# Kernel optimization log

Hardware: AMD Instinct MI355X
Metric: run time of the kernel (lower is better)

Reference implementation:

```python
import jax, jax.numpy as jnp
import numpy as np

B, T, D, H = 256, 512, 128, 256


def setup_inputs() -> dict:
    key = jax.random.key(0)
    ks = jax.random.split(key, 8)
    return {
        "x": jax.random.normal(ks[0], (B, T, D), jnp.float32),
        "m": jax.random.randint(ks[1], (B, T, D), 0, 2, jnp.int32),
        "s": jax.random.uniform(ks[2], (B, T, 1), jnp.float32),
        "kernel": jax.random.normal(ks[3], (D, 3 * H), jnp.float32) * 0.05,
        "recurrent_kernel": jax.random.normal(ks[4], (H, 3 * H), jnp.float32) * 0.05,
        "masking_kernel": jax.random.normal(ks[5], (D, 3 * H), jnp.float32) * 0.05,
        "bias": jnp.zeros((3 * H,), jnp.float32),
        "input_decay_kernel": jax.random.normal(ks[6], (D,), jnp.float32) * 0.05,
        "input_decay_bias": jnp.zeros((D,), jnp.float32),
        "hidden_decay_kernel": jax.random.normal(ks[7], (D, H), jnp.float32) * 0.05,
        "hidden_decay_bias": jnp.zeros((H,), jnp.float32),
    }


def _grud_scan(x, m, s, kernel, recurrent_kernel, masking_kernel, bias,
               input_decay_kernel, input_decay_bias,
               hidden_decay_kernel, hidden_decay_bias):
    b, t, d = x.shape
    h = recurrent_kernel.shape[0]
    mf = m.astype(x.dtype)
    mb = m > 0  # boolean mask, K.switch semantics
    # mask projection is h-independent -> hoist the big GEMM out of the scan
    mproj = jnp.einsum('btd,dk->btk', mf, masking_kernel)  # [B,T,3H]
    Kz, Kr, Kh = kernel[:, :h], kernel[:, h:2 * h], kernel[:, 2 * h:]
    Rz, Rr, Rh = recurrent_kernel[:, :h], recurrent_kernel[:, h:2 * h], recurrent_kernel[:, 2 * h:]
    bz, br, bh = bias[:h], bias[h:2 * h], bias[2 * h:]

    def step(carry, inp):
        h_tm1, x_keep, s_prev = carry
        xt, mbt, st, mpt = inp  # xt [B,D], mbt [B,D] bool, st [B,1], mpt [B,3H]
        d_t = st - s_prev  # [B,D] via broadcast
        gamma_di = jnp.exp(-jax.nn.relu(d_t * input_decay_kernel + input_decay_bias))
        gamma_dh = jnp.exp(-jax.nn.relu(d_t @ hidden_decay_kernel + hidden_decay_bias))
        x_keep_t = jnp.where(mbt, xt, x_keep)
        x_t = jnp.where(mbt, xt, gamma_di * x_keep_t)
        h_d = gamma_dh * h_tm1
        mz, mr, mh = mpt[:, :h], mpt[:, h:2 * h], mpt[:, 2 * h:]
        z_t = jax.nn.sigmoid(x_t @ Kz + h_d @ Rz + mz + bz)
        r_pre = x_t @ Kr + h_d @ Rr + mr + br  # original uses pre-activation r in hh
        hh_t = jnp.tanh(x_t @ Kh + (r_pre * h_d) @ Rh + mh + bh)
        h_t = z_t * h_tm1 + (1.0 - z_t) * hh_t
        s_keep = jnp.where(mbt, jnp.broadcast_to(st, s_prev.shape), s_prev)
        return (h_t, x_keep_t, s_keep), h_t

    init = (jnp.zeros((b, h), x.dtype), jnp.zeros((b, d), x.dtype), jnp.zeros((b, d), x.dtype))
    xs = (jnp.swapaxes(x, 0, 1), jnp.swapaxes(mb, 0, 1),
          jnp.swapaxes(s, 0, 1), jnp.swapaxes(mproj, 0, 1))
    _, hs = jax.lax.scan(step, init, xs)  # hs: [T,B,H]
    return jnp.swapaxes(hs, 0, 1)  # [B,T,H]


def reference(x, m, s, kernel, recurrent_kernel, masking_kernel, bias,
              input_decay_kernel, input_decay_bias,
              hidden_decay_kernel, hidden_decay_bias):
    return _grud_scan(x, m, s, kernel, recurrent_kernel, masking_kernel, bias,
                      input_decay_kernel, input_decay_bias,
                      hidden_decay_kernel, hidden_decay_bias)
```

## Files before the change

kernel.cpp:

```cpp
#include <hip/hip_runtime.h>
#include <hip/hip_bf16.h>
#include <cstdint>


#define Bsz 256
#define Tsz 512
#define Dsz 128
#define Hsz 256
#define BT  (Bsz * Tsz)
#define N3H 768

typedef __attribute__((ext_vector_type(8))) short   short8;
typedef __attribute__((ext_vector_type(8))) __bf16  bf16x8;
typedef __attribute__((ext_vector_type(4))) float   f32x4;

__device__ __forceinline__ unsigned short f2bf(float f) {
    union { float f; unsigned u; } v; v.f = f;
    unsigned r = v.u + 0x7fffu + ((v.u >> 16) & 1u);
    return (unsigned short)(r >> 16);
}
__device__ __forceinline__ float b2f(unsigned short u) {
    union { unsigned u; float f; } v; v.u = ((unsigned)u) << 16;
    return v.f;
}
__device__ __forceinline__ bf16x8 ld_frag(const unsigned short* p) {
    short8 v = *(const short8*)p;
    return __builtin_bit_cast(bf16x8, v);
}

__device__ __forceinline__ void barrier_lds() {
    asm volatile("s_waitcnt lgkmcnt(0)\n\ts_barrier" ::: "memory");
}

__global__ void k_pack(const float* __restrict__ kern, const float* __restrict__ maskk,
                       const float* __restrict__ rk,   const float* __restrict__ hdk,
                       unsigned short* __restrict__ KM_T, unsigned short* __restrict__ R_T,
                       unsigned short* __restrict__ W_T) {
    int i = blockIdx.x * 256 + threadIdx.x;
    if (i < N3H * 256) {
        int n = i >> 8, k = i & 255;
        float v = (k < 128) ? kern[k * N3H + n] : maskk[(k - 128) * N3H + n];
        KM_T[i] = f2bf(v);
        R_T[i]  = f2bf(rk[k * N3H + n]);
    } else {
        int j = i - N3H * 256;
        if (j < 256 * 128) {
            int n = j >> 7, k = j & 127;
            W_T[j] = f2bf(hdk[k * 256 + n]);
        }
    }
}

__global__ __launch_bounds__(256) void k_locf(
        const float* __restrict__ x, const int* __restrict__ m,
        const float* __restrict__ s, const float* __restrict__ wdi,
        const float* __restrict__ bdi,
        unsigned short* __restrict__ X2, unsigned short* __restrict__ Dt) {
    int gid = blockIdx.x * blockDim.x + threadIdx.x;
    int b = gid >> 7, d = gid & 127;
    float w  = wdi[d], bi = bdi[d];
    float x_keep = 0.f, s_prev = 0.f;
    const float* xb  = x + (size_t)b * Tsz * Dsz + d;
    const int*   mb_ = m + (size_t)b * Tsz * Dsz + d;
    const float* sb  = s + (size_t)b * Tsz;
    unsigned short* X2b = X2 + (size_t)b * Tsz * 256 + d;
    unsigned short* Dtb = Dt + (size_t)b * Tsz * 128 + d;
    for (int t0 = 0; t0 < Tsz; t0 += 4) {
        float xv[4], sv[4]; int mv[4];
#pragma unroll
        for (int u = 0; u < 4; u++) {
            xv[u] = xb[(size_t)(t0 + u) * Dsz];
            mv[u] = mb_[(size_t)(t0 + u) * Dsz];
            sv[u] = sb[t0 + u];
        }
#pragma unroll
        for (int u = 0; u < 4; u++) {
            int t = t0 + u;
            float dt  = sv[u] - s_prev;
            float gdi = __expf(-fmaxf(dt * w + bi, 0.f));
            bool  mbt = mv[u] > 0;
            if (mbt) x_keep = xv[u];
            float xe = mbt ? xv[u] : gdi * x_keep;
            if (mbt) s_prev = sv[u];
            X2b[(size_t)t * 256]       = f2bf(xe);
            X2b[(size_t)t * 256 + 128] = f2bf((float)mv[u]);
            Dtb[(size_t)t * 128]       = f2bf(dt);
        }
    }
}

template <int MODE, int K, int N>
__global__ __launch_bounds__(256) void k_gemm(
        const unsigned short* __restrict__ A, const unsigned short* __restrict__ Bt,
        const float* __restrict__ bias, unsigned short* __restrict__ C) {
    __shared__ unsigned short As[128][40];
    __shared__ unsigned short Bs[128][40];
    int m0 = blockIdx.x * 128, n0 = blockIdx.y * 128;
    int tid = threadIdx.x, lane = tid & 63, w = tid >> 6;
    int wm = w & 1, wn = w >> 1;
    int r15 = lane & 15, q = lane >> 4;
    int arow = tid >> 2, akg = tid & 3;
    f32x4 acc[4][4];
#pragma unroll
    for (int i = 0; i < 4; i++)
#pragma unroll
        for (int j = 0; j < 4; j++) acc[i][j] = f32x4{0.f, 0.f, 0.f, 0.f};

    for (int kk = 0; kk < K; kk += 32) {
        short8 av0 = *(const short8*)(A  + (size_t)(m0 + arow)      * K + kk + akg * 8);
        short8 av1 = *(const short8*)(A  + (size_t)(m0 + arow + 64) * K + kk + akg * 8);
        short8 bv0 = *(const short8*)(Bt + (size_t)(n0 + arow)      * K + kk + akg * 8);
        short8 bv1 = *(const short8*)(Bt + (size_t)(n0 + arow + 64) * K + kk + akg * 8);
        *(short8*)&As[arow][akg * 8]      = av0;
        *(short8*)&As[arow + 64][akg * 8] = av1;
        *(short8*)&Bs[arow][akg * 8]      = bv0;
        *(short8*)&Bs[arow + 64][akg * 8] = bv1;
        __syncthreads();
        bf16x8 af[4], bf[4];
#pragma unroll
        for (int i = 0; i < 4; i++) af[i] = ld_frag(&As[wm * 64 + i * 16 + r15][q * 8]);
#pragma unroll
        for (int j = 0; j < 4; j++) bf[j] = ld_frag(&Bs[wn * 64 + j * 16 + r15][q * 8]);
#pragma unroll
        for (int i = 0; i < 4; i++)
#pragma unroll
            for (int j = 0; j < 4; j++)
                acc[i][j] = __builtin_amdgcn_mfma_f32_16x16x32_bf16(af[i], bf[j], acc[i][j], 0, 0, 0);
        __syncthreads();
    }
#pragma unroll
    for (int i = 0; i < 4; i++)
#pragma unroll
        for (int j = 0; j < 4; j++) {
            int col = n0 + wn * 64 + j * 16 + r15;
            float bs = bias[col];
#pragma unroll
            for (int rg = 0; rg < 4; rg++) {
                int row = m0 + wm * 64 + i * 16 + q * 4 + rg;
                float v = acc[i][j][rg] + bs;
                if (MODE == 1) v = __expf(-fmaxf(v, 0.f));
                C[(size_t)row * N + col] = f2bf(v);
            }
        }
}

__global__ __launch_bounds__(512, 2) void k_scan(
        const unsigned short* __restrict__ Apre, const unsigned short* __restrict__ G,
        const unsigned short* __restrict__ R_T, float* __restrict__ out) {
    int b = blockIdx.x;
    int tid = threadIdx.x, lane = tid & 63, w = tid >> 6;
    int r15 = lane & 15, q = lane >> 4;

    __shared__ float h_lds[256];
    __shared__ float hd_f32[256];
    __shared__ float z_buf[256];
    __shared__ __align__(16) unsigned short hd_bf[256];
    __shared__ __align__(16) unsigned short u_bf[256];
    __shared__ __align__(16) unsigned short ap_l[2][768];
    __shared__ __align__(16) unsigned short g_l[2][256];

    bf16x8 fzr[4][8];
    bf16x8 fh[2][8];
#pragma unroll
    for (int nt = 0; nt < 4; nt++) {
        const unsigned short* base = R_T + (size_t)(w * 64 + nt * 16 + r15) * 256 + q * 8;
#pragma unroll
        for (int kt = 0; kt < 8; kt++) {
            fzr[nt][kt] = ld_frag(base + kt * 32);
            asm volatile("" : "+v"(fzr[nt][kt]));
        }
    }
#pragma unroll
    for (int nt = 0; nt < 2; nt++) {
        const unsigned short* base = R_T + (size_t)(512 + w * 32 + nt * 16 + r15) * 256 + q * 8;
#pragma unroll
        for (int kt = 0; kt < 8; kt++) {
            fh[nt][kt] = ld_frag(base + kt * 32);
            asm volatile("" : "+v"(fh[nt][kt]));
        }
    }

    if (tid < 256) { h_lds[tid] = 0.f; hd_f32[tid] = 0.f; hd_bf[tid] = 0; }

    const unsigned short* aprow = Apre + (size_t)b * Tsz * N3H;
    const unsigned short* grow  = G    + (size_t)b * Tsz * 256;

    if (tid < 192)      *(uint2*)&ap_l[0][tid * 4]         = *(const uint2*)(aprow + tid * 4);
    else if (tid < 384) *(uint2*)&ap_l[1][(tid-192) * 4]   = *(const uint2*)(aprow + N3H + (tid-192) * 4);
    else if (tid < 448) *(uint2*)&g_l[0][(tid-384) * 4]    = *(const uint2*)(grow + (tid-384) * 4);
    else                *(uint2*)&g_l[1][(tid-448) * 4]    = *(const uint2*)(grow + 256 + (tid-448) * 4);
    __syncthreads();

    float* outb = out + (size_t)b * Tsz * 256;
    for (int t = 0; t < Tsz; t++) {
        int buf = t & 1;
        int tp2 = (t + 2 < Tsz) ? t + 2 : Tsz - 1;
        unsigned pf;
        if (tid < 384) pf = *(const unsigned*)(aprow + (size_t)tp2 * N3H + tid * 2);
        else           pf = *(const unsigned*)(grow  + (size_t)tp2 * 256 + (tid - 384) * 2);

        f32x4 acc[4];
#pragma unroll
        for (int nt = 0; nt < 4; nt++) acc[nt] = f32x4{0.f, 0.f, 0.f, 0.f};
#pragma unroll
        for (int kt = 0; kt < 8; kt++) {
            bf16x8 afr = ld_frag(&hd_bf[kt * 32 + q * 8]);
#pragma unroll
            for (int nt = 0; nt < 4; nt++)
                acc[nt] = __builtin_amdgcn_mfma_f32_16x16x32_bf16(afr, fzr[nt][kt], acc[nt], 0, 0, 0);
        }
        {
            int c = w * 64 + q * 16 + r15;
            float pre = acc[q][0] + b2f(ap_l[buf][c]);
            if (w < 4) {
                z_buf[c] = 1.f / (1.f + __expf(-pre));
            } else {
                int uc = c - 256;
                u_bf[uc] = f2bf(pre * hd_f32[uc]);
            }
        }
        barrier_lds();

        f32x4 acch[2];
#pragma unroll
        for (int nt = 0; nt < 2; nt++) acch[nt] = f32x4{0.f, 0.f, 0.f, 0.f};
#pragma unroll
        for (int kt = 0; kt < 8; kt++) {
            bf16x8 afr = ld_frag(&u_bf[kt * 32 + q * 8]);
#pragma unroll
            for (int nt = 0; nt < 2; nt++)
                acch[nt] = __builtin_amdgcn_mfma_f32_16x16x32_bf16(afr, fh[nt][kt], acch[nt], 0, 0, 0);
        }
        if (lane < 32) {
            int ch = w * 32 + q * 16 + r15;
            float pre = acch[q][0] + b2f(ap_l[buf][512 + ch]);
            float e2 = __expf(2.f * pre);
            float hh = 1.f - 2.f / (e2 + 1.f);
            float z  = z_buf[ch];
            float hn = z * h_lds[ch] + (1.f - z) * hh;
            h_lds[ch] = hn;
            outb[(size_t)t * 256 + ch] = hn;
            float hdn = b2f(g_l[buf ^ 1][ch]) * hn;
            hd_f32[ch] = hdn;
            hd_bf[ch]  = f2bf(hdn);
        }
        barrier_lds();

        if (tid < 384) *(unsigned*)&ap_l[buf][tid * 2] = pf;
        else           *(unsigned*)&g_l[buf][(tid - 384) * 2] = pf;
    }
}

extern "C" void kernel_launch(void* const* d_in, const int* in_sizes, int n_in,
                              void* d_out, int out_size, void* d_ws, size_t ws_size,
                              hipStream_t stream) {
    const float* x    = (const float*)d_in[0];
    const int*   m    = (const int*)  d_in[1];
    const float* s    = (const float*)d_in[2];
    const float* kern = (const float*)d_in[3];
    const float* rk   = (const float*)d_in[4];
    const float* mk   = (const float*)d_in[5];
    const float* bias = (const float*)d_in[6];
    const float* wdi  = (const float*)d_in[7];
    const float* bdi  = (const float*)d_in[8];
    const float* hdk  = (const float*)d_in[9];
    const float* hdb  = (const float*)d_in[10];
    float* out = (float*)d_out;

    char* ws = (char*)d_ws;
    size_t off = 0;
    auto alloc = [&](size_t bytes) -> void* {
        void* p = ws + off; off += (bytes + 255) & ~(size_t)255; return p;
    };
    unsigned short* X2   = (unsigned short*)alloc((size_t)BT * 256 * 2);
    unsigned short* Dt   = (unsigned short*)alloc((size_t)BT * 128 * 2);
    unsigned short* Apre = (unsigned short*)alloc((size_t)BT * N3H * 2);
    unsigned short* Gm   = (unsigned short*)alloc((size_t)BT * 256 * 2);
    unsigned short* KM_T = (unsigned short*)alloc((size_t)N3H * 256 * 2);
    unsigned short* R_T  = (unsigned short*)alloc((size_t)N3H * 256 * 2);
    unsigned short* W_T  = (unsigned short*)alloc((size_t)256 * 128 * 2);
    (void)ws_size; (void)in_sizes; (void)n_in; (void)out_size;

    k_pack<<<dim3((N3H * 256 + 256 * 128 + 255) / 256), dim3(256), 0, stream>>>(
        kern, mk, rk, hdk, KM_T, R_T, W_T);
    k_locf<<<dim3(Bsz * Dsz / 256), dim3(256), 0, stream>>>(x, m, s, wdi, bdi, X2, Dt);
    k_gemm<0, 256, N3H><<<dim3(BT / 128, N3H / 128), dim3(256), 0, stream>>>(X2, KM_T, bias, Apre);
    k_gemm<1, 128, 256><<<dim3(BT / 128, 256 / 128), dim3(256), 0, stream>>>(Dt, W_T, hdb, Gm);
    k_scan<<<dim3(Bsz), dim3(512), 0, stream>>>(Apre, Gm, R_T, out);
}
```

Baseline: 1.117 ms.

## Remap z/r weight columns per wave so gate state stays in registers

Reassigns the recurrent z and r weight fragments so each wave owns matching z and r columns alongside its candidate-gate columns. The hidden state, decayed state and z gate can then live in registers instead of shared memory, which removes the z_buf, h_lds and hd_f32 round trips and cuts LDS traffic in the serial per-timestep loop. In exchange, every lane now computes both sigmoid values redundantly, and the MFMA accumulator element used for each column relies on the lane layout the new code assumes.

```diff
diff --git a/kernel.cpp b/kernel.cpp
--- a/kernel.cpp
+++ b/kernel.cpp
@@ -151,9 +151,6 @@
     int tid = threadIdx.x, lane = tid & 63, w = tid >> 6;
     int r15 = lane & 15, q = lane >> 4;
 
-    __shared__ float h_lds[256];
-    __shared__ float hd_f32[256];
-    __shared__ float z_buf[256];
     __shared__ __align__(16) unsigned short hd_bf[256];
     __shared__ __align__(16) unsigned short u_bf[256];
     __shared__ __align__(16) unsigned short ap_l[2][768];
@@ -163,7 +160,9 @@
     bf16x8 fh[2][8];
 #pragma unroll
     for (int nt = 0; nt < 4; nt++) {
-        const unsigned short* base = R_T + (size_t)(w * 64 + nt * 16 + r15) * 256 + q * 8;
+        int col = (nt < 2) ? (w * 32 + nt * 16 + r15)
+                           : (256 + w * 32 + (nt - 2) * 16 + r15);
+        const unsigned short* base = R_T + (size_t)col * 256 + q * 8;
 #pragma unroll
         for (int kt = 0; kt < 8; kt++) {
             fzr[nt][kt] = ld_frag(base + kt * 32);
@@ -180,7 +179,7 @@
         }
     }
 
-    if (tid < 256) { h_lds[tid] = 0.f; hd_f32[tid] = 0.f; hd_bf[tid] = 0; }
+    if (tid < 256) hd_bf[tid] = 0;
 
     const unsigned short* aprow = Apre + (size_t)b * Tsz * N3H;
     const unsigned short* grow  = G    + (size_t)b * Tsz * 256;
@@ -190,6 +189,10 @@
     else if (tid < 448) *(uint2*)&g_l[0][(tid-384) * 4]    = *(const uint2*)(grow + (tid-384) * 4);
     else                *(uint2*)&g_l[1][(tid-448) * 4]    = *(const uint2*)(grow + 256 + (tid-448) * 4);
     __syncthreads();
+
+    int c0 = w * 32 + r15;
+    float h0 = 0.f, h1 = 0.f;
+    float hd0 = 0.f, hd1 = 0.f;
 
     float* outb = out + (size_t)b * Tsz * 256;
     for (int t = 0; t < Tsz; t++) {
@@ -209,16 +212,13 @@
             for (int nt = 0; nt < 4; nt++)
                 acc[nt] = __builtin_amdgcn_mfma_f32_16x16x32_bf16(afr, fzr[nt][kt], acc[nt], 0, 0, 0);
         }
-        {
-            int c = w * 64 + q * 16 + r15;
-            float pre = acc[q][0] + b2f(ap_l[buf][c]);
-            if (w < 4) {
-                z_buf[c] = 1.f / (1.f + __expf(-pre));
-            } else {
-                int uc = c - 256;
-                u_bf[uc] = f2bf(pre * hd_f32[uc]);
-            }
-        }
+        float pz0 = acc[0][0] + b2f(ap_l[buf][c0]);
+        float pz1 = acc[1][0] + b2f(ap_l[buf][c0 + 16]);
+        float pr0 = acc[2][0] + b2f(ap_l[buf][256 + c0]);
+        float pr1 = acc[3][0] + b2f(ap_l[buf][256 + c0 + 16]);
+        float u0 = pr0 * hd0;
+        float u1 = pr1 * hd1;
+        if (q < 2) u_bf[c0 + q * 16] = f2bf(q == 0 ? u0 : u1);
         barrier_lds();
 
         f32x4 acch[2];
@@ -231,19 +231,22 @@
             for (int nt = 0; nt < 2; nt++)
                 acch[nt] = __builtin_amdgcn_mfma_f32_16x16x32_bf16(afr, fh[nt][kt], acch[nt], 0, 0, 0);
         }
-        if (lane < 32) {
-            int ch = w * 32 + q * 16 + r15;
-            float pre = acch[q][0] + b2f(ap_l[buf][512 + ch]);
-            float e2 = __expf(2.f * pre);
-            float hh = 1.f - 2.f / (e2 + 1.f);
-            float z  = z_buf[ch];
-            float hn = z * h_lds[ch] + (1.f - z) * hh;
-            h_lds[ch] = hn;
-            outb[(size_t)t * 256 + ch] = hn;
-            float hdn = b2f(g_l[buf ^ 1][ch]) * hn;
-            hd_f32[ch] = hdn;
-            hd_bf[ch]  = f2bf(hdn);
-        }
+        float z0 = 1.f / (1.f + __expf(-pz0));
+        float z1 = 1.f / (1.f + __expf(-pz1));
+        float ph0 = acch[0][0] + b2f(ap_l[buf][512 + c0]);
+        float ph1 = acch[1][0] + b2f(ap_l[buf][512 + c0 + 16]);
+        float e0 = __expf(2.f * ph0), e1 = __expf(2.f * ph1);
+        float hh0 = 1.f - 2.f / (e0 + 1.f);
+        float hh1 = 1.f - 2.f / (e1 + 1.f);
+        float hn0 = z0 * h0 + (1.f - z0) * hh0;
+        float hn1 = z1 * h1 + (1.f - z1) * hh1;
+        h0 = hn0; h1 = hn1;
+        if (q < 2) outb[(size_t)t * 256 + c0 + q * 16] = (q == 0 ? hn0 : hn1);
+        float g0 = b2f(g_l[buf ^ 1][c0]);
+        float g1 = b2f(g_l[buf ^ 1][c0 + 16]);
+        hd0 = g0 * hn0;
+        hd1 = g1 * hn1;
+        if (q < 2) hd_bf[c0 + q * 16] = f2bf(q == 0 ? hd0 : hd1);
         barrier_lds();
 
         if (tid < 384) *(unsigned*)&ap_l[buf][tid * 2] = pf;
```

Result: slower. 1.143 ms (+2.4%).
